# Kernel optimization log

Hardware: AMD Instinct MI355X
Metric: run time of the kernel (lower is better)

## Reference

```python
import jax, jax.numpy as jnp
import numpy as np

B, L, D, H = 16, 1024, 768, 12
PHD = D // H  # per-head dim = 64


def setup_inputs() -> dict:
    key = jax.random.key(0)
    ks = jax.random.split(key, 6)
    s = 0.02  # small init scale (xavier-like magnitude)
    return {
        "embeddings": jax.random.normal(ks[0], (B, L, D), jnp.float32),
        "pre_w": jax.random.normal(ks[1], (D, D), jnp.float32) * s,
        "pre_b": jnp.zeros((D,), jnp.float32),
        "psfs": jax.random.normal(ks[2], (H, 2 * L - 1, PHD), jnp.float32) * s,
        "post_w": jax.random.normal(ks[3], (D, D), jnp.float32) * s,
        "post_b": jnp.zeros((D,), jnp.float32),
        "sparse_mat": jax.random.normal(ks[4], (L, L), jnp.float32) * s,
        "ln_g": jnp.ones((D,), jnp.float32),
        "ln_b": jnp.zeros((D,), jnp.float32),
    }


def _spectral_norm(W, n_iters=1, eps=1e-12):
    # torch spectral_norm: power iteration with detached u, v; sigma = u^T W v
    u = jnp.ones((W.shape[0],), W.dtype) / jnp.sqrt(jnp.asarray(W.shape[0], W.dtype))
    for _ in range(n_iters):
        v = W.T @ u
        v = v / (jnp.linalg.norm(v) + eps)
        u = W @ v
        u = u / (jnp.linalg.norm(u) + eps)
    u = jax.lax.stop_gradient(u)
    v = jax.lax.stop_gradient(v)
    sigma = u @ (W @ v)
    return W / sigma


def reference(embeddings, pre_w, pre_b, psfs, post_w, post_b, sparse_mat, ln_g, ln_b):
    # pre-projection
    x = embeddings @ pre_w.T + pre_b                       # (B, L, D)
    # zero-pad along seq to 2L-1 and split heads
    xp = jnp.pad(x, ((0, 0), (0, L - 1), (0, 0)))          # (B, 2L-1, D)
    xp = xp.reshape(B, 2 * L - 1, H, PHD).transpose(0, 2, 1, 3)  # (B, H, 2L-1, d)
    # causal PSF mask: keep first L taps, zero the rest (zeros still enter softmax, as in torch)
    causal = (jnp.arange(2 * L - 1) < L)[None, :, None]
    psf = jnp.where(causal, psfs, 0.0)                     # (H, 2L-1, d)
    psf = jax.nn.softmax(psf, axis=1)
    # 2D circular convolution via FFT over (seq, head_dim)
    conv = jnp.fft.ifftn(jnp.fft.fftn(psf, axes=(1, 2))[None] * jnp.fft.fftn(xp, axes=(2, 3)), axes=(2, 3))
    conv = jnp.real(conv)[:, :, :L, :]                     # (B, H, L, d)
    conv = jax.nn.gelu(conv, approximate=False).transpose(0, 2, 1, 3).reshape(B, L, D)
    conv_emb = conv @ post_w.T + post_b
    # sparse branch: spectrally-normalized, causal-masked dense mixing matrix
    sp = jnp.tril(_spectral_norm(sparse_mat))              # (L, L)
    sparse_emb = jnp.einsum('st,btd->bsd', sp, x)
    # dropout is identity (eval), keep_prob = 1.0; residual + LayerNorm(eps=1e-12)
    y = conv_emb + sparse_emb + embeddings
    mu = jnp.mean(y, axis=-1, keepdims=True)
    var = jnp.mean((y - mu) ** 2, axis=-1, keepdims=True)
    return (y - mu) * jax.lax.rsqrt(var + 1e-12) * ln_g + ln_b
```

## Files before the change

kernel.cpp:

```cpp
#include <hip/hip_runtime.h>
#include <math.h>

#define Bn 16
#define Ln 1024
#define Dn 768
#define Hn 12
#define PHDn 64
#define NK 33
#define NHK (Hn * NK)
#define TWOPI_64 0.09817477042468103f

typedef short s16x8 __attribute__((ext_vector_type(8)));
typedef float f32x4 __attribute__((ext_vector_type(4)));
typedef unsigned short u16x4 __attribute__((ext_vector_type(4)));

__device__ __forceinline__ unsigned short f2bf(float f) {
    unsigned int u = __float_as_uint(f);
    unsigned int r = (u + 0x7FFFu + ((u >> 16) & 1u)) >> 16;
    return (unsigned short)r;
}
__device__ __forceinline__ float bf2f(unsigned short s) {
    unsigned int u = ((unsigned int)s) << 16;
    return __uint_as_float(u);
}
__device__ __forceinline__ float2 cmul(float2 a, float2 b) {
    return make_float2(a.x * b.x - a.y * b.y, a.x * b.y + a.y * b.x);
}
__device__ __forceinline__ float2 cadd(float2 a, float2 b) { return make_float2(a.x + b.x, a.y + b.y); }
__device__ __forceinline__ float2 csub(float2 a, float2 b) { return make_float2(a.x - b.x, a.y - b.y); }
__device__ __forceinline__ unsigned int packbf(float re, float im) {
    return (unsigned int)f2bf(re) | ((unsigned int)f2bf(im) << 16);
}
__device__ __forceinline__ float2 unpackbf(unsigned int v) {
    return make_float2(bf2f((unsigned short)(v & 0xffff)), bf2f((unsigned short)(v >> 16)));
}

#define SW(j) ((j) ^ (((j) >> 2) & 12) ^ (((j) >> 6) & 3))
#define PD(j) ((j) + ((j) >> 4))

static const size_t O_P    = 0;
static const size_t O_PSFH = 786432;
static const size_t O_PART = 1376256;
static const size_t O_QH   = 1597440;
static const size_t O_X    = 1598240;
static const size_t O_XH   = 14181152;
static const size_t O_YH   = 27157280;
static const size_t O_SPE  = 40146080;
static const size_t O_V    = 52728992;
static const size_t O_UR   = 52730016;
static const size_t O_SIG  = 52731040;

__global__ __launch_bounds__(256) void k_psf_softmax(const float* __restrict__ psfs,
                                                     float* __restrict__ p,
                                                     float* __restrict__ q) {
    int he = blockIdx.x;
    int h = he >> 6, e = he & 63;
    int tid = threadIdx.x;
    float ev[4];
    float s = 0.f;
#pragma unroll
    for (int i = 0; i < 4; ++i) {
        int t = tid + 256 * i;
        float v = psfs[((size_t)h * 2047 + t) * 64 + e];
        ev[i] = expf(v);
        s += ev[i];
    }
    __shared__ float red[256];
    red[tid] = s; __syncthreads();
    for (int st = 128; st > 0; st >>= 1) {
        if (tid < st) red[tid] += red[tid + st];
        __syncthreads();
    }
    float denom = red[0] + 1023.0f;
    float inv = 1.0f / denom;
#pragma unroll
    for (int i = 0; i < 4; ++i) {
        int t = tid + 256 * i;
        p[((size_t)h * 1024 + t) * 64 + e] = ev[i] * inv;
    }
    if (tid == 0) q[he] = inv;
}

__global__ __launch_bounds__(256) void k_psf_dft(const float* __restrict__ p,
                                                 float* __restrict__ psfh) {
    int blk = blockIdx.x;
    int h = blk >> 8, tb = blk & 255;
    int t0 = tb * 4;
    int tid = threadIdx.x;
    int w = tid >> 6, lane = tid & 63;
    __shared__ float pv[4][64], cc[64], ssn[64];
    if (tid < 64) {
        float ang = TWOPI_64 * tid;
        cc[tid] = cosf(ang); ssn[tid] = sinf(ang);
    }
    pv[w][lane] = p[((size_t)h * 1024 + t0 + w) * 64 + lane];
    __syncthreads();
    if (lane < NK) {
        float re = 0.f, im = 0.f;
#pragma unroll 8
        for (int e = 0; e < 64; ++e) {
            int j = (lane * e) & 63;
            float v = pv[w][e];
            re += v * cc[j];
            im -= v * ssn[j];
        }
        size_t o = (((size_t)h * NK + lane) * 1024 + t0 + w) * 2;
        psfh[o] = re; psfh[o + 1] = im;
    }
}

__global__ __launch_bounds__(64) void k_q_dft(const float* __restrict__ q,
                                              float* __restrict__ qh) {
    int h = blockIdx.x;
    int tid = threadIdx.x;
    __shared__ float qv[64], cc[64], ssn[64];
    qv[tid] = q[h * 64 + tid];
    float ang = TWOPI_64 * tid;
    cc[tid] = cosf(ang); ssn[tid] = sinf(ang);
    __syncthreads();
    if (tid < NK) {
        float re = 0.f, im = 0.f;
        for (int e = 0; e < 64; ++e) {
            int j = (tid * e) & 63;
            re += qv[e] * cc[j];
            im -= qv[e] * ssn[j];
        }
        qh[(h * NK + tid) * 2] = re;
        qh[(h * NK + tid) * 2 + 1] = im;
    }
}

__device__ __forceinline__ void build_twiddles(float2* tw, int tid) {
#pragma unroll
    for (int it = 0; it < 2; ++it) {
        int j = tid + it * 256;
        float a = (float)j * 3.0679615757712823e-3f;
        float sv, cv;
        __sincosf(a, &sv, &cv);
        tw[j] = make_float2(cv, -sv);
    }
}

__device__ __forceinline__ void fft_pair(const float2* __restrict__ X,
                                         float2* __restrict__ Y,
                                         const float2* __restrict__ tw,
                                         int tid, int m) {
#pragma unroll
    for (int it = 0; it < 2; ++it) {
        int i = tid + it * 256;
        int r = i & (m - 1);
        int am = i - r;
        float2 w1 = tw[am];
        float2 w1b = make_float2(w1.y, -w1.x);
        float2 w2 = cmul(w1, w1);
        float2 x0 = X[SW(i)], x1 = X[SW(i + 512)], x2 = X[SW(i + 1024)], x3 = X[SW(i + 1536)];
        float2 y0 = cadd(x0, x2);
        float2 y1 = cmul(csub(x0, x2), w1);
        float2 y2 = cadd(x1, x3);
        float2 y3 = cmul(csub(x1, x3), w1b);
        int o = 4 * am + r;
        Y[SW(o)] = cadd(y0, y2);
        Y[SW(o + m)] = cadd(y1, y3);
        Y[SW(o + 2 * m)] = cmul(csub(y0, y2), w2);
        Y[SW(o + 3 * m)] = cmul(csub(y1, y3), w2);
    }
}

__global__ __launch_bounds__(256) void k_tap_fft(const float* __restrict__ psfh,
                                                 const float* __restrict__ qh,
                                                 float* __restrict__ phf) {
    __shared__ float2 A[2048], B[2048], tw[512];
    int hk = blockIdx.x, tid = threadIdx.x;
    build_twiddles(tw, tid);
    float2 qv = make_float2(qh[hk * 2], qh[hk * 2 + 1]);
    const float2* Pg = (const float2*)(psfh + (size_t)hk * 2048);
    __syncthreads();
#pragma unroll
    for (int it = 0; it < 2; ++it) {
        int i = tid + it * 256;
        float2 x0 = Pg[i], x1 = Pg[i + 512];
        float2 x2 = (i == 0) ? make_float2(0.f, 0.f) : qv;
        float2 x3 = qv;
        float2 w1 = tw[i];
        float2 w1b = make_float2(w1.y, -w1.x);
        float2 w2 = cmul(w1, w1);
        float2 y0 = cadd(x0, x2);
        float2 y1 = cmul(csub(x0, x2), w1);
        float2 y2 = cadd(x1, x3);
        float2 y3 = cmul(csub(x1, x3), w1b);
        int o = 4 * i;
        A[SW(o)] = cadd(y0, y2);
        A[SW(o + 1)] = cadd(y1, y3);
        A[SW(o + 2)] = cmul(csub(y0, y2), w2);
        A[SW(o + 3)] = cmul(csub(y1, y3), w2);
    }
    __syncthreads();
    fft_pair(A, B, tw, tid, 4);   __syncthreads();
    fft_pair(B, A, tw, tid, 16);  __syncthreads();
    fft_pair(A, B, tw, tid, 64);  __syncthreads();
    fft_pair(B, A, tw, tid, 256); __syncthreads();
    float2* out = (float2*)(phf + (size_t)hk * 4096);
#pragma unroll
    for (int it = 0; it < 4; ++it) {
        int t = tid + it * 256;
        float2 lo = A[SW(t)], hi = A[SW(t + 1024)];
        out[t] = cadd(lo, hi);
        out[t + 1024] = csub(lo, hi);
    }
}

__device__ __forceinline__ void triple_tail(float2 z0, float2 z1, float2 z2, float2 z3,
                                            float2 zz0, float2 zz1, float2 zz2, float2 zz3,
                                            float2 w2, float2 w4, float2* o) {
    float2 w2b = make_float2(w2.y, -w2.x);
    float2 a0 = cadd(z0, z2),   a2 = cmul(csub(z0, z2), w2);
    float2 b0 = cadd(z1, z3),   b2 = cmul(csub(z1, z3), w2b);
    float2 a1 = cadd(zz0, zz2), a3 = cmul(csub(zz0, zz2), w2);
    float2 b1 = cadd(zz1, zz3), b3 = cmul(csub(zz1, zz3), w2b);
    o[0] = cadd(a0, b0); o[4] = cmul(csub(a0, b0), w4);
    o[1] = cadd(a1, b1); o[5] = cmul(csub(a1, b1), w4);
    o[2] = cadd(a2, b2); o[6] = cmul(csub(a2, b2), w4);
    o[3] = cadd(a3, b3); o[7] = cmul(csub(a3, b3), w4);
}

__device__ __forceinline__ void fft_triple(const float2* x, float2 w10, float2 w11, float2* o) {
    float2 w10b = make_float2(w10.y, -w10.x), w11b = make_float2(w11.y, -w11.x);
    float2 w2 = cmul(w10, w10), w4 = cmul(w2, w2);
    float2 z0 = cadd(x[0], x[4]), z1 = cadd(x[1], x[5]);
    float2 z2 = cadd(x[2], x[6]), z3 = cadd(x[3], x[7]);
    float2 zz0 = cmul(csub(x[0], x[4]), w10);
    float2 zz1 = cmul(csub(x[1], x[5]), w11);
    float2 zz2 = cmul(csub(x[2], x[6]), w10b);
    float2 zz3 = cmul(csub(x[3], x[7]), w11b);
    triple_tail(z0, z1, z2, z3, zz0, zz1, zz2, zz3, w2, w4, o);
}

__global__ __launch_bounds__(256) void k_conv_fft(const unsigned int* __restrict__ XHb,
                                                  const float* __restrict__ PHF,
                                                  unsigned int* __restrict__ YHb) {
    __shared__ float2 S[2176], tw[512];
    int bhk = blockIdx.x, tid = threadIdx.x;
    int hk = bhk % NHK;
    build_twiddles(tw, tid);
    const unsigned int* Xg = XHb + (size_t)bhk * 1024;
    float2 x[8], o[8];
#pragma unroll
    for (int k = 0; k < 4; ++k) x[k] = unpackbf(Xg[tid + 256 * k]);
    __syncthreads();
    {
        float2 w10 = tw[tid], w11 = tw[tid + 256];
        float2 w10b = make_float2(w10.y, -w10.x), w11b = make_float2(w11.y, -w11.x);
        float2 w2 = cmul(w10, w10), w4 = cmul(w2, w2);
        float2 zz0 = cmul(x[0], w10), zz1 = cmul(x[1], w11);
        float2 zz2 = cmul(x[2], w10b), zz3 = cmul(x[3], w11b);
        triple_tail(x[0], x[1], x[2], x[3], zz0, zz1, zz2, zz3, w2, w4, o);
    }
#pragma unroll
    for (int k = 0; k < 8; ++k) S[PD(8 * tid + k)] = o[k];
    __syncthreads();
    {
        int r = tid & 7, am = tid - r;
#pragma unroll
        for (int k = 0; k < 8; ++k) x[k] = S[PD(tid + 256 * k)];
        __syncthreads();
        fft_triple(x, tw[am], tw[am + 256], o);
        int base = 8 * am + r;
#pragma unroll
        for (int k = 0; k < 8; ++k) S[PD(base + 8 * k)] = o[k];
    }
    __syncthreads();
    {
        int r = tid & 63, am = tid - r;
#pragma unroll
        for (int k = 0; k < 8; ++k) x[k] = S[PD(tid + 256 * k)];
        __syncthreads();
        fft_triple(x, tw[am], tw[am + 256], o);
        int base = 8 * am + r;
#pragma unroll
        for (int k = 0; k < 8; ++k) S[PD(base + 64 * k)] = o[k];
    }
    __syncthreads();
    const float2* P = (const float2*)(PHF + (size_t)hk * 4096);
    float2 v[8];
#pragma unroll
    for (int it = 0; it < 2; ++it) {
        int i2 = tid + 256 * it;
        float2 g0 = S[PD(i2)], g1 = S[PD(i2 + 512)], g2 = S[PD(i2 + 1024)], g3 = S[PD(i2 + 1536)];
        float2 y0 = cadd(g0, g2), y1 = csub(g0, g2);
        float2 y2 = cadd(g1, g3);
        float2 d13 = csub(g1, g3);
        float2 y3 = make_float2(d13.y, -d13.x);
        float2 F0 = cadd(y0, y2);
        float2 F1 = cadd(y1, y3);
        float2 F2 = csub(y0, y2);
        float2 F3 = csub(y1, y3);
        float2 V0 = cmul(F0, P[i2]);
        float2 V1 = cmul(F1, P[i2 + 512]);
        float2 V2 = cmul(F2, P[i2 + 1024]);
        float2 V3 = cmul(F3, P[i2 + 1536]);
        v[it]     = make_float2(V0.x, -V0.y);
        v[it + 2] = make_float2(V1.x, -V1.y);
        v[it + 4] = make_float2(V2.x, -V2.y);
        v[it + 6] = make_float2(V3.x, -V3.y);
    }
    __syncthreads();
    fft_triple(v, tw[tid], tw[tid + 256], o);
#pragma unroll
    for (int k = 0; k < 8; ++k) S[PD(8 * tid + k)] = o[k];
    __syncthreads();
    {
        int r = tid & 7, am = tid - r;
#pragma unroll
        for (int k = 0; k < 8; ++k) x[k] = S[PD(tid + 256 * k)];
        __syncthreads();
        fft_triple(x, tw[am], tw[am + 256], o);
        int base = 8 * am + r;
#pragma unroll
        for (int k = 0; k < 8; ++k) S[PD(base + 8 * k)] = o[k];
    }
    __syncthreads();
    {
        int r = tid & 63, am = tid - r;
#pragma unroll
        for (int k = 0; k < 8; ++k) x[k] = S[PD(tid + 256 * k)];
        __syncthreads();
        fft_triple(x, tw[am], tw[am + 256], o);
        int base = 8 * am + r;
#pragma unroll
        for (int k = 0; k < 8; ++k) S[PD(base + 64 * k)] = o[k];
    }
    __syncthreads();
    unsigned int* Yg = YHb + (size_t)bhk * 1024;
    const float inv_n = 1.0f / 2048.0f;
#pragma unroll
    for (int it = 0; it < 2; ++it) {
        int i2 = tid + 256 * it;
        float2 g0 = S[PD(i2)], g1 = S[PD(i2 + 512)], g2 = S[PD(i2 + 1024)], g3 = S[PD(i2 + 1536)];
        float2 s02 = cadd(g0, g2), d02 = csub(g0, g2);
        float2 s13 = cadd(g1, g3);
        float2 d13 = csub(g1, g3);
        float2 mj13 = make_float2(d13.y, -d13.x);
        float2 o0 = cadd(s02, s13);
        float2 o1 = cadd(d02, mj13);
        Yg[i2] = packbf(o0.x * inv_n, -o0.y * inv_n);
        Yg[i2 + 512] = packbf(o1.x * inv_n, -o1.y * inv_n);
    }
}

__global__ __launch_bounds__(64) void k_build_wf1(unsigned short* __restrict__ W) {
    int m = blockIdx.x;
    int d = threadIdx.x;
    float val = 0.f;
    if (m < 66) {
        int k = m >> 1, od = m & 1;
        int j = (k * d) & 63;
        float ang = TWOPI_64 * (float)j;
        val = od ? -sinf(ang) : cosf(ang);
    }
    W[m * 64 + d] = f2bf(val);
}

__global__ __launch_bounds__(64) void k_build_wi1(unsigned short* __restrict__ W) {
    int m = blockIdx.x;
    int c = threadIdx.x;
    float val = 0.f;
    if (m < 64) {
        int d = m;
        int k, od;
        float ck;
        if (c == 0)      { k = 0;  od = 0; ck = 1.f / 64.f; }
        else if (c == 1) { k = 32; od = 0; ck = 1.f / 64.f; }
        else             { k = c >> 1; od = c & 1; ck = 2.f / 64.f; }
        int j = (k * d) & 63;
        float ang = TWOPI_64 * (float)j;
        val = od ? -sinf(ang) * ck : cosf(ang) * ck;
    }
    W[m * 64 + c] = f2bf(val);
}

__device__ __forceinline__ void mfma_core64(const unsigned short* __restrict__ gA0,
                                            const unsigned short* __restrict__ gB0,
                                            int nkt,
                                            unsigned short* __restrict__ As,
                                            unsigned short* __restrict__ Bs,
                                            int tid, int lane, int wr, int wc,
                                            f32x4 acc[4][4]) {
    int r0 = tid >> 1, hs = (tid & 1) << 2;
    int wbase = r0 * 64;
    int swr = r0 & 7;
    int kg = lane >> 4, cl = lane & 15;
    int fra[8], frb[8];
#pragma unroll
    for (int kk = 0; kk < 2; ++kk)
#pragma unroll
        for (int i = 0; i < 4; ++i) {
            int ra = wr * 64 + i * 16 + cl;
            fra[kk * 4 + i] = ra * 64 + (((kk * 4 + kg) ^ (ra & 7)) << 3);
            int rb = wc * 64 + i * 16 + cl;
            frb[kk * 4 + i] = rb * 64 + (((kk * 4 + kg) ^ (rb & 7)) << 3);
        }
    s16x8 a[4], b[4];
#pragma unroll
    for (int l = 0; l < 4; ++l) {
        a[l] = *(const s16x8*)(gA0 + l * 8);
        b[l] = *(const s16x8*)(gB0 + l * 8);
    }
    for (int kt = 0; kt < nkt; ++kt) {
        __syncthreads();
#pragma unroll
        for (int l = 0; l < 4; ++l) {
            *(s16x8*)&As[wbase + (((hs + l) ^ swr) << 3)] = a[l];
            *(s16x8*)&Bs[wbase + (((hs + l) ^ swr) << 3)] = b[l];
        }
        __syncthreads();
        if (kt + 1 < nkt) {
            size_t ko = (size_t)(kt + 1) * 64;
#pragma unroll
            for (int l = 0; l < 4; ++l) {
                a[l] = *(const s16x8*)(gA0 + ko + l * 8);
                b[l] = *(const s16x8*)(gB0 + ko + l * 8);
            }
        }
#pragma unroll
        for (int kk = 0; kk < 2; ++kk) {
            s16x8 af[4], bfr[4];
#pragma unroll
            for (int i = 0; i < 4; ++i) af[i] = *(const s16x8*)&As[fra[kk * 4 + i]];
#pragma unroll
            for (int i = 0; i < 4; ++i) bfr[i] = *(const s16x8*)&Bs[frb[kk * 4 + i]];
#pragma unroll
            for (int mi = 0; mi < 4; ++mi)
#pragma unroll
                for (int ni = 0; ni < 4; ++ni)
                    acc[mi][ni] = __builtin_amdgcn_mfma_f32_16x16x32_bf16(af[mi], bfr[ni], acc[mi][ni], 0, 0, 0);
        }
    }
}

__global__ __launch_bounds__(512) void k_mfma_proj(const unsigned short* __restrict__ A,
                                                   const unsigned short* __restrict__ W,
                                                   const float* __restrict__ bias,
                                                   unsigned short* __restrict__ C) {
    const int K = Dn, N = Dn;
    int n0 = blockIdx.x * 256, m0 = blockIdx.y * 128;
    int tid = threadIdx.x;
    int lane = tid & 63, wave = tid >> 6;
    int wr = wave >> 2, wc = wave & 3;
    __shared__ __align__(16) unsigned short As[8192], Bs[16384];
    f32x4 acc[4][4] = {};
    int ra0 = tid >> 2, sa0 = (tid & 3) * 2;
    int rb0 = tid >> 1, sb0 = (tid & 1) * 4;
    const unsigned short* gA = A + (size_t)(m0 + ra0) * K + sa0 * 8;
    const unsigned short* gB = W + (size_t)(n0 + rb0) * K + sb0 * 8;
    int kg = lane >> 4, cl = lane & 15;
    int fra[8], frb[8];
#pragma unroll
    for (int kk = 0; kk < 2; ++kk)
#pragma unroll
        for (int i = 0; i < 4; ++i) {
            int ra = wr * 64 + i * 16 + cl;
            fra[kk * 4 + i] = ra * 64 + (((kk * 4 + kg) ^ (ra & 7)) << 3);
            int rb = wc * 64 + i * 16 + cl;
            frb[kk * 4 + i] = rb * 64 + (((kk * 4 + kg) ^ (rb & 7)) << 3);
        }
    s16x8 a[2], b[4];
#pragma unroll
    for (int l = 0; l < 2; ++l) a[l] = *(const s16x8*)(gA + l * 8);
#pragma unroll
    for (int l = 0; l < 4; ++l) b[l] = *(const s16x8*)(gB + l * 8);
    const int nkt = K >> 6;
    for (int kt = 0; kt < nkt; ++kt) {
        __syncthreads();
#pragma unroll
        for (int l = 0; l < 2; ++l)
            *(s16x8*)&As[ra0 * 64 + (((sa0 + l) ^ (ra0 & 7)) << 3)] = a[l];
#pragma unroll
        for (int l = 0; l < 4; ++l)
            *(s16x8*)&Bs[rb0 * 64 + (((sb0 + l) ^ (rb0 & 7)) << 3)] = b[l];
        __syncthreads();
        if (kt + 1 < nkt) {
            size_t ko = (size_t)(kt + 1) * 64;
#pragma unroll
            for (int l = 0; l < 2; ++l) a[l] = *(const s16x8*)(gA + ko + l * 8);
#pragma unroll
            for (int l = 0; l < 4; ++l) b[l] = *(const s16x8*)(gB + ko + l * 8);
        }
#pragma unroll
        for (int kk = 0; kk < 2; ++kk) {
            s16x8 af[4], bfr[4];
#pragma unroll
            for (int i = 0; i < 4; ++i) af[i] = *(const s16x8*)&As[fra[kk * 4 + i]];
#pragma unroll
            for (int i = 0; i < 4; ++i) bfr[i] = *(const s16x8*)&Bs[frb[kk * 4 + i]];
#pragma unroll
            for (int mi = 0; mi < 4; ++mi)
#pragma unroll
                for (int ni = 0; ni < 4; ++ni)
                    acc[mi][ni] = __builtin_amdgcn_mfma_f32_16x16x32_bf16(af[mi], bfr[ni], acc[mi][ni], 0, 0, 0);
        }
    }
#pragma unroll
    for (int ni = 0; ni < 4; ++ni) {
        int gn = n0 + wc * 64 + ni * 16 + cl;
        float bv = bias[gn];
#pragma unroll
        for (int mi = 0; mi < 4; ++mi) {
            int gm = m0 + wr * 64 + mi * 16 + kg * 4;
            f32x4 v = acc[mi][ni];
#pragma unroll
            for (int ri = 0; ri < 4; ++ri)
                C[(size_t)(gm + ri) * N + gn] = f2bf(v[ri] + bv);
        }
    }
}

__global__ __launch_bounds__(256) void k_mfma_dft_h(const unsigned short* __restrict__ Wf1,
                                                    const unsigned short* __restrict__ Xb,
                                                    unsigned int* __restrict__ XHb) {
    int n0 = blockIdx.x * 128;
    int h = blockIdx.y;
    int tid = threadIdx.x;
    int lane = tid & 63, wave = tid >> 6;
    int wr = wave >> 1, wc = wave & 1;
    __shared__ __align__(16) unsigned short As[8192], Bs[8192];
    f32x4 acc[4][4] = {};
    int r0 = tid >> 1, hs = (tid & 1) << 2;
    const unsigned short* gA0 = Wf1 + r0 * 64 + hs * 8;
    const unsigned short* gB0 = Xb + (size_t)(n0 + r0) * Dn + h * 64 + hs * 8;
    mfma_core64(gA0, gB0, 1, As, Bs, tid, lane, wr, wc, acc);
    int kg = lane >> 4, cl = lane & 15;
#pragma unroll
    for (int ni = 0; ni < 4; ++ni) {
        int gn = n0 + wc * 64 + ni * 16 + cl;
        int b = gn >> 10, u = gn & 1023;
#pragma unroll
        for (int mi = 0; mi < 4; ++mi) {
            int gmb = wr * 64 + mi * 16 + kg * 4;
            f32x4 v = acc[mi][ni];
#pragma unroll
            for (int rp = 0; rp < 2; ++rp) {
                int m = gmb + rp * 2;
                if (m < 66) {
                    size_t plane = (size_t)(b * Hn + h) * NK + (m >> 1);
                    XHb[plane * 1024 + u] = packbf(v[rp * 2], v[rp * 2 + 1]);
                }
            }
        }
    }
}

__global__ __launch_bounds__(256) void k_mfma_idft_h(const unsigned int* __restrict__ YHb,
                                                     const unsigned short* __restrict__ Wi1,
                                                     unsigned short* __restrict__ G) {
    int m0 = blockIdx.x * 128;
    int h = blockIdx.y;
    int b = m0 >> 10, u0 = m0 & 1023;
    int tid = threadIdx.x;
    int lane = tid & 63, wave = tid >> 6;
    int wr = wave >> 1, wc = wave & 1;
    __shared__ __align__(16) unsigned short As[8192], Bs[8192];
    int planeBase = (b * Hn + h) * NK;
#pragma unroll
    for (int i = 0; i < 17; ++i) {
        int idx = tid + i * 256;
        if (idx < 4224) {
            int k = idx >> 7, uo = idx & 127;
            unsigned int v = YHb[(size_t)(planeBase + k) * 1024 + u0 + uo];
            unsigned short lo = (unsigned short)(v & 0xffff);
            unsigned short hi = (unsigned short)(v >> 16);
            int sw = uo & 7;
            int rb = uo * 64;
            if (k == 0) {
                As[rb + (sw << 3) + 0] = lo;
            } else if (k == 32) {
                As[rb + (sw << 3) + 1] = lo;
            } else {
                int c0 = 2 * k, c1 = 2 * k + 1;
                As[rb + (((c0 >> 3) ^ sw) << 3) + (c0 & 7)] = lo;
                As[rb + (((c1 >> 3) ^ sw) << 3) + (c1 & 7)] = hi;
            }
        }
    }
    {
        int r0 = tid >> 1, hs = (tid & 1) << 2;
        int swr = r0 & 7;
        const unsigned short* gB0 = Wi1 + r0 * 64 + hs * 8;
#pragma unroll
        for (int l = 0; l < 4; ++l)
            *(s16x8*)&Bs[r0 * 64 + (((hs + l) ^ swr) << 3)] = *(const s16x8*)(gB0 + l * 8);
    }
    __syncthreads();
    f32x4 acc[4][4] = {};
    int kg = lane >> 4, cl = lane & 15;
#pragma unroll
    for (int kk = 0; kk < 2; ++kk) {
        s16x8 af[4], bfr[4];
#pragma unroll
        for (int i = 0; i < 4; ++i) {
            int ra = wr * 64 + i * 16 + cl;
            af[i] = *(const s16x8*)&As[ra * 64 + (((kk * 4 + kg) ^ (ra & 7)) << 3)];
            int rbw = wc * 64 + i * 16 + cl;
            bfr[i] = *(const s16x8*)&Bs[rbw * 64 + (((kk * 4 + kg) ^ (rbw & 7)) << 3)];
        }
#pragma unroll
        for (int mi = 0; mi < 4; ++mi)
#pragma unroll
            for (int ni = 0; ni < 4; ++ni)
                acc[mi][ni] = __builtin_amdgcn_mfma_f32_16x16x32_bf16(af[mi], bfr[ni], acc[mi][ni], 0, 0, 0);
    }
#pragma unroll
    for (int ni = 0; ni < 4; ++ni) {
        int gn = wc * 64 + ni * 16 + cl;
        if (gn < 64) {
#pragma unroll
            for (int mi = 0; mi < 4; ++mi) {
                int gm = m0 + wr * 64 + mi * 16 + kg * 4;
                f32x4 v = acc[mi][ni];
#pragma unroll
                for (int ri = 0; ri < 4; ++ri) {
                    float c = v[ri];
                    float g = c * 0.5f * (1.0f + erff(c * 0.70710678118f));
                    G[(size_t)(gm + ri) * Dn + h * 64 + gn] = f2bf(g);
                }
            }
        }
    }
}

__global__ __launch_bounds__(256) void k_mfma_sparse(const unsigned short* __restrict__ SP,
                                                     const unsigned short* __restrict__ XT,
                                                     const float* __restrict__ sigbuf,
                                                     unsigned short* __restrict__ C) {
    int bx = blockIdx.x;
    int mt = bx & 7, nt = (bx >> 3) % 6, b = bx / 48;
    int m0 = mt * 128, n0 = nt * 128;
    const unsigned short* Xb = XT + (size_t)b * Dn * Ln;
    unsigned short* Cb = C + (size_t)b * Ln * Dn;
    int tid = threadIdx.x;
    int lane = tid & 63, wave = tid >> 6;
    int wr = wave >> 1, wc = wave & 1;
    __shared__ __align__(16) unsigned short As[8192], Bs[8192];
    f32x4 acc[4][4] = {};
    int r0 = tid >> 1, hs = (tid & 1) << 2;
    const unsigned short* gA0 = SP + (size_t)(m0 + r0) * Ln + hs * 8;
    const unsigned short* gB0 = Xb + (size_t)(n0 + r0) * Ln + hs * 8;
    mfma_core64(gA0, gB0, 2 * mt + 2, As, Bs, tid, lane, wr, wc, acc);
    float invs = sigbuf[0];
    int kg = lane >> 4, cl = lane & 15;
#pragma unroll
    for (int ni = 0; ni < 4; ++ni) {
        int gn = n0 + wc * 64 + ni * 16 + cl;
#pragma unroll
        for (int mi = 0; mi < 4; ++mi) {
            int gm = m0 + wr * 64 + mi * 16 + kg * 4;
            f32x4 v = acc[mi][ni];
#pragma unroll
            for (int ri = 0; ri < 4; ++ri)
                Cb[(size_t)(gm + ri) * Dn + gn] = f2bf(v[ri] * invs);
        }
    }
}

__global__ __launch_bounds__(256) void k_cvt_bf16(const float* __restrict__ in,
                                                  unsigned short* __restrict__ out, int n4) {
    int i = blockIdx.x * 256 + threadIdx.x;
    if (i < n4) {
        float4 v = ((const float4*)in)[i];
        u16x4 o;
        o[0] = f2bf(v.x); o[1] = f2bf(v.y); o[2] = f2bf(v.z); o[3] = f2bf(v.w);
        *(u16x4*)&out[(size_t)i * 4] = o;
    }
}

__global__ __launch_bounds__(256) void k_cvt_sp(const float* __restrict__ SP,
                                                unsigned short* __restrict__ O) {
    int s = blockIdx.x;
    int t0 = threadIdx.x * 4;
    float4 v = *(const float4*)&SP[(size_t)s * 1024 + t0];
    u16x4 o;
    o[0] = (t0 + 0 <= s) ? f2bf(v.x) : 0;
    o[1] = (t0 + 1 <= s) ? f2bf(v.y) : 0;
    o[2] = (t0 + 2 <= s) ? f2bf(v.z) : 0;
    o[3] = (t0 + 3 <= s) ? f2bf(v.w) : 0;
    *(u16x4*)&O[(size_t)s * 1024 + t0] = o;
}

__global__ __launch_bounds__(256) void k_transpose_x(const unsigned short* __restrict__ X,
                                                     unsigned short* __restrict__ XT) {
    int d0 = blockIdx.x * 64, t0 = blockIdx.y * 64, b = blockIdx.z;
    const unsigned short* Xb = X + (size_t)b * Ln * Dn;
    unsigned short* Tb = XT + (size_t)b * Dn * Ln;
    __shared__ unsigned short tile[64 * 65];
    int tx = threadIdx.x & 63, ty = threadIdx.x >> 6;
#pragma unroll
    for (int i = 0; i < 16; ++i) {
        int t = ty + i * 4;
        tile[t * 65 + tx] = Xb[(size_t)(t0 + t) * Dn + d0 + tx];
    }
    __syncthreads();
#pragma unroll
    for (int i = 0; i < 16; ++i) {
        int d = ty + i * 4;
        Tb[(size_t)(d0 + d) * Ln + t0 + tx] = tile[tx * 65 + d];
    }
}

__global__ __launch_bounds__(256) void k_sn_colsum(const float* __restrict__ Wm,
                                                   float* __restrict__ partial) {
    int b = blockIdx.x;
    int tid = threadIdx.x;
    int c0 = tid * 4;
    float4 s = make_float4(0.f, 0.f, 0.f, 0.f);
#pragma unroll
    for (int i = 0; i < 16; ++i) {
        float4 v = *(const float4*)&Wm[(size_t)(b * 16 + i) * 1024 + c0];
        s.x += v.x; s.y += v.y; s.z += v.z; s.w += v.w;
    }
    *(float4*)&partial[(size_t)b * 1024 + c0] = s;
}

__global__ __launch_bounds__(1024) void k_sn_v2(const float* __restrict__ partial,
                                                float* __restrict__ v) {
    int j = threadIdx.x;
    float s = 0.f;
#pragma unroll 8
    for (int i = 0; i < 64; ++i) s += partial[(size_t)i * 1024 + j];
    s *= 0.03125f;
    __shared__ float red[1024];
    red[j] = s * s; __syncthreads();
    for (int st = 512; st > 0; st >>= 1) {
        if (j < st) red[j] += red[j + st];
        __syncthreads();
    }
    float nrm = sqrtf(red[0]);
    v[j] = s / (nrm + 1e-12f);
}

__global__ __launch_bounds__(64) void k_sn_u(const float* __restrict__ Wm,
                                             const float* __restrict__ v,
                                             float* __restrict__ ur) {
    int i = blockIdx.x;
    int lane = threadIdx.x;
    float s = 0.f;
    for (int j = lane; j < 1024; j += 64) s += Wm[(size_t)i * 1024 + j] * v[j];
#pragma unroll
    for (int off = 32; off > 0; off >>= 1) s += __shfl_down(s, off);
    if (lane == 0) ur[i] = s;
}

__global__ __launch_bounds__(1024) void k_sn_sigma(const float* __restrict__ ur,
                                                   float* __restrict__ sig) {
    int i = threadIdx.x;
    __shared__ float red[1024];
    float u = ur[i];
    red[i] = u * u; __syncthreads();
    for (int st = 512; st > 0; st >>= 1) {
        if (i < st) red[i] += red[i + st];
        __syncthreads();
    }
    if (i == 0) {
        float ss = red[0];
        float sigma = ss / (sqrtf(ss) + 1e-12f);
        sig[0] = 1.0f / sigma;
    }
}

__global__ __launch_bounds__(256) void k_final_ln(const unsigned short* __restrict__ CE,
                                                  const unsigned short* __restrict__ SE,
                                                  const unsigned short* __restrict__ EMB,
                                                  const float* __restrict__ g,
                                                  const float* __restrict__ be,
                                                  float* __restrict__ out) {
    int r = blockIdx.x;
    int tid = threadIdx.x;
    float y[3];
    float s = 0.f;
#pragma unroll
    for (int i = 0; i < 3; ++i) {
        int o = tid + i * 256;
        size_t idx = (size_t)r * 768 + o;
        y[i] = bf2f(CE[idx]) + bf2f(SE[idx]) + bf2f(EMB[idx]);
        s += y[i];
    }
    __shared__ float red[256];
    red[tid] = s; __syncthreads();
    for (int st = 128; st > 0; st >>= 1) {
        if (tid < st) red[tid] += red[tid + st];
        __syncthreads();
    }
    float mu = red[0] * (1.f / 768.f);
    __syncthreads();
    float vs = 0.f;
#pragma unroll
    for (int i = 0; i < 3; ++i) { float d = y[i] - mu; vs += d * d; }
    red[tid] = vs; __syncthreads();
    for (int st = 128; st > 0; st >>= 1) {
        if (tid < st) red[tid] += red[tid + st];
        __syncthreads();
    }
    float var = red[0] * (1.f / 768.f);
    float rstd = rsqrtf(var + 1e-12f);
#pragma unroll
    for (int i = 0; i < 3; ++i) {
        int o = tid + i * 256;
        size_t idx = (size_t)r * 768 + o;
        out[idx] = (y[i] - mu) * rstd * g[o] + be[o];
    }
}

extern "C" void kernel_launch(void* const* d_in, const int* in_sizes, int n_in,
                              void* d_out, int out_size, void* d_ws, size_t ws_size,
                              hipStream_t stream) {
    const float* emb     = (const float*)d_in[0];
    const float* pre_w   = (const float*)d_in[1];
    const float* pre_b   = (const float*)d_in[2];
    const float* psfs    = (const float*)d_in[3];
    const float* post_w  = (const float*)d_in[4];
    const float* post_b  = (const float*)d_in[5];
    const float* spmat   = (const float*)d_in[6];
    const float* ln_g    = (const float*)d_in[7];
    const float* ln_b    = (const float*)d_in[8];
    float* out = (float*)d_out;
    float* ws = (float*)d_ws;

    float* p      = ws + O_P;
    float* psfh   = ws + O_PSFH;
    float* part   = ws + O_PART;
    float* qh     = ws + O_QH;
    float* q      = ws + O_SIG + 8;
    float* phf    = ws + O_SPE;
    float* v      = ws + O_V;
    float* urw    = ws + O_UR;
    float* sig    = ws + O_SIG;

    unsigned int* XHb = (unsigned int*)(ws + O_XH);
    unsigned int* YHb = (unsigned int*)(ws + O_YH + 6291456);
    unsigned short* emb_bf    = (unsigned short*)(ws + O_YH);
    unsigned short* x_bf      = (unsigned short*)(ws + O_X);
    unsigned short* Wf1       = (unsigned short*)(ws + O_X + 6291456);
    unsigned short* Wi1       = (unsigned short*)(ws + O_X + 6295552);
    unsigned short* xT_bf     = (unsigned short*)(ws + O_XH);
    unsigned short* CE_bf     = (unsigned short*)(ws + O_XH + 6488064);
    unsigned short* spe_bf    = (unsigned short*)(ws + O_SPE);
    unsigned short* G_bf      = (unsigned short*)(ws + O_SPE + 3145728);
    unsigned short* SP_bf     = (unsigned short*)(ws + O_P);
    unsigned short* pre_w_bf  = (unsigned short*)(ws + O_PSFH);
    unsigned short* post_w_bf = (unsigned short*)(ws + O_PSFH + 294912);

    k_psf_softmax<<<Hn * 64, 256, 0, stream>>>(psfs, p, q);
    k_psf_dft<<<Hn * 256, 256, 0, stream>>>(p, psfh);
    k_q_dft<<<Hn, 64, 0, stream>>>(q, qh);
    k_tap_fft<<<NHK, 256, 0, stream>>>(psfh, qh, phf);

    k_sn_colsum<<<64, 256, 0, stream>>>(spmat, part);
    k_sn_v2<<<1, 1024, 0, stream>>>(part, v);
    k_sn_u<<<1024, 64, 0, stream>>>(spmat, v, urw);
    k_sn_sigma<<<1, 1024, 0, stream>>>(urw, sig);

    k_cvt_sp<<<1024, 256, 0, stream>>>(spmat, SP_bf);
    k_cvt_bf16<<<576, 256, 0, stream>>>(pre_w, pre_w_bf, 147456);
    k_cvt_bf16<<<576, 256, 0, stream>>>(post_w, post_w_bf, 147456);
    k_cvt_bf16<<<12288, 256, 0, stream>>>(emb, emb_bf, 3145728);
    k_build_wf1<<<128, 64, 0, stream>>>(Wf1);
    k_build_wi1<<<128, 64, 0, stream>>>(Wi1);

    k_mfma_proj<<<dim3(3, 128), 512, 0, stream>>>(emb_bf, pre_w_bf, pre_b, x_bf);

    k_mfma_dft_h<<<dim3(128, Hn), 256, 0, stream>>>(Wf1, x_bf, XHb);

    k_conv_fft<<<Bn * NHK, 256, 0, stream>>>(XHb, phf, YHb);

    k_mfma_idft_h<<<dim3(128, Hn), 256, 0, stream>>>(YHb, Wi1, G_bf);

    k_transpose_x<<<dim3(12, 16, Bn), 256, 0, stream>>>(x_bf, xT_bf);

    k_mfma_proj<<<dim3(3, 128), 512, 0, stream>>>(G_bf, post_w_bf, post_b, CE_bf);

    k_mfma_sparse<<<768, 256, 0, stream>>>(SP_bf, xT_bf, sig, spe_bf);

    k_final_ln<<<Bn * Ln, 256, 0, stream>>>(CE_bf, spe_bf, emb_bf, ln_g, ln_b, out);
}
```

Baseline: 304.6 us.

## Fuse x transpose into pre-projection epilogue and widen sparse GEMM tiles

The pre-projection GEMM epilogue now also writes a transposed copy of x (4 contiguous bf16 per lane), so the separate transpose kernel is removed. The sparse causal GEMM moves from 128x128 tiles with 256 threads to 128x256 tiles with 512 threads and an inline register-prefetch loop, halving the block count. The two DFT-matrix build kernels are merged into one launch. The transposed stores are small scattered writes and may be poorly coalesced. The xT buffer gets its own workspace region, so it can be written early without clashing with XH.

```diff
diff --git a/kernel.cpp b/kernel.cpp
--- a/kernel.cpp
+++ b/kernel.cpp
@@ -43,7 +43,8 @@
 static const size_t O_PART = 1376256;
 static const size_t O_QH   = 1597440;
 static const size_t O_X    = 1598240;
-static const size_t O_XH   = 14181152;
+static const size_t O_XT   = 7897888;
+static const size_t O_XH   = 14189344;
 static const size_t O_YH   = 27157280;
 static const size_t O_SPE  = 40146080;
 static const size_t O_V    = 52728992;
@@ -347,35 +348,35 @@
     }
 }
 
-__global__ __launch_bounds__(64) void k_build_wf1(unsigned short* __restrict__ W) {
-    int m = blockIdx.x;
-    int d = threadIdx.x;
-    float val = 0.f;
-    if (m < 66) {
-        int k = m >> 1, od = m & 1;
-        int j = (k * d) & 63;
-        float ang = TWOPI_64 * (float)j;
-        val = od ? -sinf(ang) : cosf(ang);
-    }
-    W[m * 64 + d] = f2bf(val);
-}
-
-__global__ __launch_bounds__(64) void k_build_wi1(unsigned short* __restrict__ W) {
+__global__ __launch_bounds__(64) void k_build_w(unsigned short* __restrict__ Wf,
+                                                unsigned short* __restrict__ Wi) {
     int m = blockIdx.x;
     int c = threadIdx.x;
-    float val = 0.f;
-    if (m < 64) {
-        int d = m;
-        int k, od;
-        float ck;
-        if (c == 0)      { k = 0;  od = 0; ck = 1.f / 64.f; }
-        else if (c == 1) { k = 32; od = 0; ck = 1.f / 64.f; }
-        else             { k = c >> 1; od = c & 1; ck = 2.f / 64.f; }
-        int j = (k * d) & 63;
-        float ang = TWOPI_64 * (float)j;
-        val = od ? -sinf(ang) * ck : cosf(ang) * ck;
-    }
-    W[m * 64 + c] = f2bf(val);
+    if (m < 128) {
+        float val = 0.f;
+        if (m < 66) {
+            int k = m >> 1, od = m & 1;
+            int j = (k * c) & 63;
+            float ang = TWOPI_64 * (float)j;
+            val = od ? -sinf(ang) : cosf(ang);
+        }
+        Wf[m * 64 + c] = f2bf(val);
+    } else {
+        int mm = m - 128;
+        float val = 0.f;
+        if (mm < 64) {
+            int d = mm;
+            int k, od;
+            float ck;
+            if (c == 0)      { k = 0;  od = 0; ck = 1.f / 64.f; }
+            else if (c == 1) { k = 32; od = 0; ck = 1.f / 64.f; }
+            else             { k = c >> 1; od = c & 1; ck = 2.f / 64.f; }
+            int j = (k * d) & 63;
+            float ang = TWOPI_64 * (float)j;
+            val = od ? -sinf(ang) * ck : cosf(ang) * ck;
+        }
+        Wi[mm * 64 + c] = f2bf(val);
+    }
 }
 
 __device__ __forceinline__ void mfma_core64(const unsigned short* __restrict__ gA0,
@@ -440,7 +441,8 @@
 __global__ __launch_bounds__(512) void k_mfma_proj(const unsigned short* __restrict__ A,
                                                    const unsigned short* __restrict__ W,
                                                    const float* __restrict__ bias,
-                                                   unsigned short* __restrict__ C) {
+                                                   unsigned short* __restrict__ C,
+                                                   unsigned short* __restrict__ XT) {
     const int K = Dn, N = Dn;
     int n0 = blockIdx.x * 256, m0 = blockIdx.y * 128;
     int tid = threadIdx.x;
@@ -499,6 +501,7 @@
                     acc[mi][ni] = __builtin_amdgcn_mfma_f32_16x16x32_bf16(af[mi], bfr[ni], acc[mi][ni], 0, 0, 0);
         }
     }
+    int b0 = m0 >> 10;
 #pragma unroll
     for (int ni = 0; ni < 4; ++ni) {
         int gn = n0 + wc * 64 + ni * 16 + cl;
@@ -507,9 +510,17 @@
         for (int mi = 0; mi < 4; ++mi) {
             int gm = m0 + wr * 64 + mi * 16 + kg * 4;
             f32x4 v = acc[mi][ni];
-#pragma unroll
-            for (int ri = 0; ri < 4; ++ri)
-                C[(size_t)(gm + ri) * N + gn] = f2bf(v[ri] + bv);
+            u16x4 o;
+#pragma unroll
+            for (int ri = 0; ri < 4; ++ri) {
+                unsigned short bfv = f2bf(v[ri] + bv);
+                o[ri] = bfv;
+                C[(size_t)(gm + ri) * N + gn] = bfv;
+            }
+            if (XT) {
+                int t = gm & 1023;
+                *(u16x4*)&XT[((size_t)b0 * Dn + gn) * Ln + t] = o;
+            }
         }
     }
 }
@@ -627,26 +638,72 @@
     }
 }
 
-__global__ __launch_bounds__(256) void k_mfma_sparse(const unsigned short* __restrict__ SP,
+__global__ __launch_bounds__(512) void k_mfma_sparse(const unsigned short* __restrict__ SP,
                                                      const unsigned short* __restrict__ XT,
                                                      const float* __restrict__ sigbuf,
                                                      unsigned short* __restrict__ C) {
     int bx = blockIdx.x;
-    int mt = bx & 7, nt = (bx >> 3) % 6, b = bx / 48;
-    int m0 = mt * 128, n0 = nt * 128;
+    int mt = bx & 7, nt = (bx >> 3) % 3, b = bx / 24;
+    int m0 = mt * 128, n0 = nt * 256;
     const unsigned short* Xb = XT + (size_t)b * Dn * Ln;
     unsigned short* Cb = C + (size_t)b * Ln * Dn;
     int tid = threadIdx.x;
     int lane = tid & 63, wave = tid >> 6;
-    int wr = wave >> 1, wc = wave & 1;
-    __shared__ __align__(16) unsigned short As[8192], Bs[8192];
+    int wr = wave >> 2, wc = wave & 3;
+    __shared__ __align__(16) unsigned short As[8192], Bs[16384];
     f32x4 acc[4][4] = {};
-    int r0 = tid >> 1, hs = (tid & 1) << 2;
-    const unsigned short* gA0 = SP + (size_t)(m0 + r0) * Ln + hs * 8;
-    const unsigned short* gB0 = Xb + (size_t)(n0 + r0) * Ln + hs * 8;
-    mfma_core64(gA0, gB0, 2 * mt + 2, As, Bs, tid, lane, wr, wc, acc);
+    int ra0 = tid >> 2, sa0 = (tid & 3) * 2;
+    int rb0 = tid >> 1, sb0 = (tid & 1) * 4;
+    const unsigned short* gA = SP + (size_t)(m0 + ra0) * Ln + sa0 * 8;
+    const unsigned short* gB = Xb + (size_t)(n0 + rb0) * Ln + sb0 * 8;
+    int kg = lane >> 4, cl = lane & 15;
+    int fra[8], frb[8];
+#pragma unroll
+    for (int kk = 0; kk < 2; ++kk)
+#pragma unroll
+        for (int i = 0; i < 4; ++i) {
+            int ra = wr * 64 + i * 16 + cl;
+            fra[kk * 4 + i] = ra * 64 + (((kk * 4 + kg) ^ (ra & 7)) << 3);
+            int rb = wc * 64 + i * 16 + cl;
+            frb[kk * 4 + i] = rb * 64 + (((kk * 4 + kg) ^ (rb & 7)) << 3);
+        }
+    s16x8 a[2], b2[4];
+#pragma unroll
+    for (int l = 0; l < 2; ++l) a[l] = *(const s16x8*)(gA + l * 8);
+#pragma unroll
+    for (int l = 0; l < 4; ++l) b2[l] = *(const s16x8*)(gB + l * 8);
+    int nkt = 2 * mt + 2;
+    for (int kt = 0; kt < nkt; ++kt) {
+        __syncthreads();
+#pragma unroll
+        for (int l = 0; l < 2; ++l)
+            *(s16x8*)&As[ra0 * 64 + (((sa0 + l) ^ (ra0 & 7)) << 3)] = a[l];
+#pragma unroll
+        for (int l = 0; l < 4; ++l)
+            *(s16x8*)&Bs[rb0 * 64 + (((sb0 + l) ^ (rb0 & 7)) << 3)] = b2[l];
+        __syncthreads();
+        if (kt + 1 < nkt) {
+            size_t ko = (size_t)(kt + 1) * 64;
+#pragma unroll
+            for (int l = 0; l < 2; ++l) a[l] = *(const s16x8*)(gA + ko + l * 8);
+#pragma unroll
+            for (int l = 0; l < 4; ++l) b2[l] = *(const s16x8*)(gB + ko + l * 8);
+        }
+#pragma unroll
+        for (int kk = 0; kk < 2; ++kk) {
+            s16x8 af[4], bfr[4];
+#pragma unroll
+            for (int i = 0; i < 4; ++i) af[i] = *(const s16x8*)&As[fra[kk * 4 + i]];
+#pragma unroll
+            for (int i = 0; i < 4; ++i) bfr[i] = *(const s16x8*)&Bs[frb[kk * 4 + i]];
+#pragma unroll
+            for (int mi = 0; mi < 4; ++mi)
+#pragma unroll
+                for (int ni = 0; ni < 4; ++ni)
+                    acc[mi][ni] = __builtin_amdgcn_mfma_f32_16x16x32_bf16(af[mi], bfr[ni], acc[mi][ni], 0, 0, 0);
+        }
+    }
     float invs = sigbuf[0];
-    int kg = lane >> 4, cl = lane & 15;
 #pragma unroll
     for (int ni = 0; ni < 4; ++ni) {
         int gn = n0 + wc * 64 + ni * 16 + cl;
@@ -683,26 +740,6 @@
     o[2] = (t0 + 2 <= s) ? f2bf(v.z) : 0;
     o[3] = (t0 + 3 <= s) ? f2bf(v.w) : 0;
     *(u16x4*)&O[(size_t)s * 1024 + t0] = o;
-}
-
-__global__ __launch_bounds__(256) void k_transpose_x(const unsigned short* __restrict__ X,
-                                                     unsigned short* __restrict__ XT) {
-    int d0 = blockIdx.x * 64, t0 = blockIdx.y * 64, b = blockIdx.z;
-    const unsigned short* Xb = X + (size_t)b * Ln * Dn;
-    unsigned short* Tb = XT + (size_t)b * Dn * Ln;
-    __shared__ unsigned short tile[64 * 65];
-    int tx = threadIdx.x & 63, ty = threadIdx.x >> 6;
-#pragma unroll
-    for (int i = 0; i < 16; ++i) {
-        int t = ty + i * 4;
-        tile[t * 65 + tx] = Xb[(size_t)(t0 + t) * Dn + d0 + tx];
-    }
-    __syncthreads();
-#pragma unroll
-    for (int i = 0; i < 16; ++i) {
-        int d = ty + i * 4;
-        Tb[(size_t)(d0 + d) * Ln + t0 + tx] = tile[tx * 65 + d];
-    }
 }
 
 __global__ __launch_bounds__(256) void k_sn_colsum(const float* __restrict__ Wm,
@@ -839,7 +876,7 @@
     unsigned short* x_bf      = (unsigned short*)(ws + O_X);
     unsigned short* Wf1       = (unsigned short*)(ws + O_X + 6291456);
     unsigned short* Wi1       = (unsigned short*)(ws + O_X + 6295552);
-    unsigned short* xT_bf     = (unsigned short*)(ws + O_XH);
+    unsigned short* xT_bf     = (unsigned short*)(ws + O_XT);
     unsigned short* CE_bf     = (unsigned short*)(ws + O_XH + 6488064);
     unsigned short* spe_bf    = (unsigned short*)(ws + O_SPE);
     unsigned short* G_bf      = (unsigned short*)(ws + O_SPE + 3145728);
@@ -861,10 +898,9 @@
     k_cvt_bf16<<<576, 256, 0, stream>>>(pre_w, pre_w_bf, 147456);
     k_cvt_bf16<<<576, 256, 0, stream>>>(post_w, post_w_bf, 147456);
     k_cvt_bf16<<<12288, 256, 0, stream>>>(emb, emb_bf, 3145728);
-    k_build_wf1<<<128, 64, 0, stream>>>(Wf1);
-    k_build_wi1<<<128, 64, 0, stream>>>(Wi1);
-
-    k_mfma_proj<<<dim3(3, 128), 512, 0, stream>>>(emb_bf, pre_w_bf, pre_b, x_bf);
+    k_build_w<<<256, 64, 0, stream>>>(Wf1, Wi1);
+
+    k_mfma_proj<<<dim3(3, 128), 512, 0, stream>>>(emb_bf, pre_w_bf, pre_b, x_bf, xT_bf);
 
     k_mfma_dft_h<<<dim3(128, Hn), 256, 0, stream>>>(Wf1, x_bf, XHb);
 
@@ -872,11 +908,9 @@
 
     k_mfma_idft_h<<<dim3(128, Hn), 256, 0, stream>>>(YHb, Wi1, G_bf);
 
-    k_transpose_x<<<dim3(12, 16, Bn), 256, 0, stream>>>(x_bf, xT_bf);
-
-    k_mfma_proj<<<dim3(3, 128), 512, 0, stream>>>(G_bf, post_w_bf, post_b, CE_bf);
-
-    k_mfma_sparse<<<768, 256, 0, stream>>>(SP_bf, xT_bf, sig, spe_bf);
+    k_mfma_proj<<<dim3(3, 128), 512, 0, stream>>>(G_bf, post_w_bf, post_b, CE_bf, nullptr);
+
+    k_mfma_sparse<<<384, 512, 0, stream>>>(SP_bf, xT_bf, sig, spe_bf);
 
     k_final_ln<<<Bn * Ln, 256, 0, stream>>>(CE_bf, spe_bf, emb_bf, ln_g, ln_b, out);
 }
```

Result: no change. 304.9 us (+0.1%).
